# Optimization experiments

Hardware: AMD Instinct MI355X
Metric: run time of the kernel (lower is better)

The kernel has to match this reference:

```python
import jax, jax.numpy as jnp
import numpy as np

B, N, NC, D, H = 2, 8192, 512, 512, 16
HD = D // H            # 32
SCALE = HD ** -0.5
EPS = 1e-6


def setup_inputs() -> dict:
    key = jax.random.key(0)
    k0, k1, k2, k3, k4 = jax.random.split(key, 5)
    return {
        "x": jax.random.normal(k0, (B, N, D), dtype=jnp.float32),
        "clusters": jax.random.normal(k1, (B, NC, D), dtype=jnp.float32),
        "Wq": jax.random.normal(k2, (D, D), dtype=jnp.float32) * 0.02,
        "Wkv": jax.random.normal(k3, (D, 2 * D), dtype=jnp.float32) * 0.02,
        "Wout": jax.random.normal(k4, (D, D), dtype=jnp.float32) * 0.02,
    }


def reference(x, clusters, Wq, Wkv, Wout):
    # projections (torch Linear without bias == matmul with weight)
    q = clusters @ Wq                      # [b, nc, d]
    kv = x @ Wkv                           # [b, n, 2d]
    # split heads: 'b n (h d) -> b h n d' and 'b n (k h d) -> k b h n d'
    q = q.reshape(B, NC, H, HD).transpose(0, 2, 1, 3)        # [b, h, nc, hd]
    kv = kv.reshape(B, N, 2, H, HD)
    k = kv[:, :, 0].transpose(0, 2, 1, 3)                    # [b, h, n, hd]
    v = kv[:, :, 1].transpose(0, 2, 1, 3)                    # [b, h, n, hd]

    attn = jnp.einsum('bhqd,bhkd->bhqk', q, k) * SCALE       # [b, h, nc, n]
    # 'soft' assignment: softmax over the CLUSTER (query) axis, dim=-2
    attn = jax.nn.softmax(attn, axis=-2)
    token_sizes = attn.sum(-1)                               # [b, h, nc]
    attn = attn / (token_sizes[..., None] + EPS)
    token_sizes = token_sizes.mean(axis=1)                   # [b, nc]

    out = jnp.einsum('bhqk,bhkd->bhqd', attn, v)             # [b, h, nc, hd]
    out = out.transpose(0, 2, 1, 3).reshape(B, NC, D)        # [b, nc, d]
    out = out @ Wout
    return out, token_sizes
```

## Files before the change

kernel.cpp:

```cpp
#include <hip/hip_runtime.h>
#include <hip/hip_bf16.h>

#define B_ 2
#define N_ 8192
#define NC_ 512
#define D_ 512
#define H_ 16
#define HD_ 32
#define SCALE_ 0.17677669529663687f
#define LOG2E_ 1.4426950408889634f
#define EPS_ 1e-6f
#define NCHUNK 32
#define CHUNK (N_ / NCHUNK)

typedef __attribute__((ext_vector_type(8))) short bf16x8_t;
typedef __attribute__((ext_vector_type(4))) short bf16x4_t;
typedef __attribute__((ext_vector_type(4))) float f32x4_t;

static __device__ __forceinline__ short f2bf(float f) {
    unsigned u = __float_as_uint(f);
    unsigned r = (u + 0x7FFFu + ((u >> 16) & 1u)) >> 16;
    return (short)r;
}

static __device__ __forceinline__ float fast_exp2(float x) {
#if __has_builtin(__builtin_amdgcn_exp2f)
    return __builtin_amdgcn_exp2f(x);
#else
    float r; asm("v_exp_f32 %0, %1" : "=v"(r) : "v"(x)); return r;
#endif
}

static __device__ __forceinline__ void gload_lds16(const short* g, void* l) {
    __builtin_amdgcn_global_load_lds(
        (const __attribute__((address_space(1))) void*)g,
        (__attribute__((address_space(3))) void*)l, 16, 0, 0);
}

__global__ __launch_bounds__(256) void cvt_bf16_kernel(
    const float* __restrict__ a, short* __restrict__ ao, int na8,
    const float* __restrict__ b, short* __restrict__ bo)
{
    int i8 = blockIdx.x * 256 + threadIdx.x;
    const float* src; short* dst;
    if (i8 < na8) { src = a + (size_t)i8 * 8; dst = ao + (size_t)i8 * 8; }
    else { size_t o = (size_t)(i8 - na8) * 8; src = b + o; dst = bo + o; }
    float4 v0 = *(const float4*)src;
    float4 v1 = *(const float4*)(src + 4);
    bf16x8_t p = {f2bf(v0.x), f2bf(v0.y), f2bf(v0.z), f2bf(v0.w),
                  f2bf(v1.x), f2bf(v1.y), f2bf(v1.z), f2bf(v1.w)};
    *(bf16x8_t*)dst = p;
}

__global__ __launch_bounds__(256) void transpose_cvt_kernel(
    const float* __restrict__ Wq, const float* __restrict__ Wkv,
    const float* __restrict__ Wout,
    short* __restrict__ WqT, short* __restrict__ WkvT, short* __restrict__ WoutT)
{
    const float* src; short* dst; int ncols;
    if (blockIdx.z == 0)      { src = Wq;   dst = WqT;   ncols = 512; }
    else if (blockIdx.z == 1) { src = Wkv;  dst = WkvT;  ncols = 1024; }
    else                      { src = Wout; dst = WoutT; ncols = 512; }
    if ((int)blockIdx.x * 32 >= ncols) return;

    __shared__ short t[32][34];
    const int c0 = blockIdx.x * 32, r0 = blockIdx.y * 32;
    const int tc = threadIdx.x & 31, tr = threadIdx.x >> 5;
#pragma unroll
    for (int i = 0; i < 4; i++) {
        int r = tr + i * 8;
        t[tc][r] = f2bf(src[(size_t)(r0 + r) * ncols + c0 + tc]);
    }
    __syncthreads();
#pragma unroll
    for (int i = 0; i < 4; i++) {
        int outr = tr + i * 8;
        dst[(size_t)(c0 + outr) * 512 + r0 + tc] = t[outr][tc];
    }
}

template <bool OUT_BF16>
__global__ __launch_bounds__(256) void gemm_bt_kernel(
    const short* __restrict__ A, const short* __restrict__ BT,
    void* __restrict__ C, int M, int N, int K, float oscale)
{
    __shared__ short As[128 * 32];
    __shared__ short Bs[128 * 32];

    const int tid = threadIdx.x;
    const int wid = tid >> 6, lane = tid & 63;
    const int l16 = lane & 15, lg = lane >> 4;
    const int wr = (wid >> 1) * 64, wc = (wid & 1) * 64;

    const int nwg = gridDim.x * gridDim.y;
    const int flat = blockIdx.y * gridDim.x + blockIdx.x;
    const int swz = (flat & 7) * (nwg >> 3) + (flat >> 3);
    const int bx = swz % gridDim.x, by = swz / gridDim.x;

    const f32x4_t zero4 = {0.f, 0.f, 0.f, 0.f};
    f32x4_t acc[4][4];
#pragma unroll
    for (int i = 0; i < 4; i++)
#pragma unroll
        for (int j = 0; j < 4; j++) acc[i][j] = zero4;

    const short* aptr = A + (size_t)(by * 128 + wid * 16 + (lane >> 2)) * K + (lane & 3) * 8;
    const short* bptr = BT + (size_t)(bx * 128 + wid * 16 + (lane >> 2)) * K + (lane & 3) * 8;
    char* al = (char*)As + wid * 1024;
    char* bl = (char*)Bs + wid * 1024;
    const size_t rstep = (size_t)64 * K;

    for (int kt = 0; kt < K; kt += 32) {
        gload_lds16(aptr + kt, al);
        gload_lds16(aptr + rstep + kt, al + 4096);
        gload_lds16(bptr + kt, bl);
        gload_lds16(bptr + rstep + kt, bl + 4096);
        __syncthreads();

        bf16x8_t bfr[4];
#pragma unroll
        for (int nf = 0; nf < 4; nf++)
            bfr[nf] = *(const bf16x8_t*)&Bs[(wc + nf * 16 + l16) * 32 + lg * 8];
#pragma unroll
        for (int mf = 0; mf < 4; mf++) {
            bf16x8_t afr = *(const bf16x8_t*)&As[(wr + mf * 16 + l16) * 32 + lg * 8];
#pragma unroll
            for (int nf = 0; nf < 4; nf++)
                acc[mf][nf] = __builtin_amdgcn_mfma_f32_16x16x32_bf16(
                    afr, bfr[nf], acc[mf][nf], 0, 0, 0);
        }
        __syncthreads();
    }

#pragma unroll
    for (int mf = 0; mf < 4; mf++) {
#pragma unroll
        for (int nf = 0; nf < 4; nf++) {
            int row0 = by * 128 + wr + mf * 16 + lg * 4;
            int col  = bx * 128 + wc + nf * 16 + l16;
#pragma unroll
            for (int r = 0; r < 4; r++) {
                float v = acc[mf][nf][r] * oscale;
                if (OUT_BF16)
                    ((short*)C)[(size_t)(row0 + r) * N + col] = f2bf(v);
                else
                    ((float*)C)[(size_t)(row0 + r) * N + col] = v;
            }
        }
    }
}

__global__ __launch_bounds__(256) void attn_kernel(
    const short* __restrict__ qb,
    const short* __restrict__ kvb,
    short* __restrict__ out_part,
    float* __restrict__ ts_part)
{
    const int chunk = blockIdx.x, h = blockIdx.y, b = blockIdx.z;
    const int tid = threadIdx.x, wid = tid >> 6, lane = tid & 63;
    const int l16 = lane & 15, lg = lane >> 4;

    __shared__ short P_lds[512 * 32];
    __shared__ short v_t[2][32][40];
    __shared__ float reds[2][2][4][16];

    bf16x8_t qf[8];
#pragma unroll
    for (int mf = 0; mf < 8; mf++) {
        int row = wid * 128 + mf * 16 + l16;
        qf[mf] = *(const bf16x8_t*)&qb[(size_t)(b * NC_ + row) * D_ + h * HD_ + lg * 8];
    }

    const f32x4_t zero4 = {0.f, 0.f, 0.f, 0.f};
    f32x4_t oacc[8][2], tsacc[8];
#pragma unroll
    for (int mf = 0; mf < 8; mf++) {
        oacc[mf][0] = zero4; oacc[mf][1] = zero4; tsacc[mf] = zero4;
    }
    bf16x8_t onesf;
#pragma unroll
    for (int j = 0; j < 8; j++) onesf[j] = (short)0x3F80;

    const short* kptr = kvb + (size_t)(b * N_ + chunk * CHUNK + l16) * (2 * D_) + h * HD_ + lg * 8;
    const int skey = tid >> 3, sd0 = (tid & 7) * 4;
    const short* vptr = kvb + (size_t)(b * N_ + chunk * CHUNK + skey) * (2 * D_) + D_ + h * HD_ + sd0;
    char* Pb = (char*)P_lds;

    for (int kt = 0; kt < CHUNK / 32; kt++) {
        const int cur = kt & 1;
        const size_t koff = (size_t)kt * 32 * (2 * D_);

        bf16x8_t kf0 = *(const bf16x8_t*)(kptr + koff);
        bf16x8_t kf1 = *(const bf16x8_t*)(kptr + koff + 16 * (2 * D_));
        bf16x4_t vv  = *(const bf16x4_t*)(vptr + koff);
        v_t[cur][sd0 + 0][skey] = vv[0];
        v_t[cur][sd0 + 1][skey] = vv[1];
        v_t[cur][sd0 + 2][skey] = vv[2];
        v_t[cur][sd0 + 3][skey] = vv[3];

#pragma unroll
        for (int half = 0; half < 2; half++) {
            f32x4_t s[8];
            bf16x8_t kf = half ? kf1 : kf0;
#pragma unroll
            for (int mf = 0; mf < 8; mf++)
                s[mf] = __builtin_amdgcn_mfma_f32_16x16x32_bf16(qf[mf], kf, zero4, 0, 0, 0);

            float sl = 0.f;
#pragma unroll
            for (int mf = 0; mf < 8; mf++)
#pragma unroll
                for (int r = 0; r < 4; r++) {
                    float e = fast_exp2(s[mf][r]);
                    s[mf][r] = e; sl += e;
                }
            sl += __shfl_xor(sl, 16, 64);
            sl += __shfl_xor(sl, 32, 64);
            if (lane < 16) reds[cur][half][wid][lane] = sl;
            __syncthreads();
            float inv = __fdividef(1.f, reds[cur][half][0][l16] + reds[cur][half][1][l16] +
                                        reds[cur][half][2][l16] + reds[cur][half][3][l16]);

            const int kbyte = (l16 & 7) * 2;
            const int ku = (l16 >> 3) + half * 2;
#pragma unroll
            for (int mf = 0; mf < 8; mf++) {
#pragma unroll
                for (int r = 0; r < 4; r++) {
                    int row = wid * 128 + mf * 16 + lg * 4 + r;
                    int x = (row >> 1) & 3;
                    int by0 = row * 64 + kbyte + (((ku ^ x) & 3) << 4);
                    *(short*)(Pb + by0) = (short)(__float_as_uint(s[mf][r] * inv) >> 16);
                }
            }
        }

        bf16x8_t v0 = *(const bf16x8_t*)&v_t[cur][l16][lg * 8];
        bf16x8_t v1 = *(const bf16x8_t*)&v_t[cur][16 + l16][lg * 8];
#pragma unroll
        for (int mf = 0; mf < 8; mf++) {
            int row = wid * 128 + mf * 16 + l16;
            bf16x8_t pa = *(const bf16x8_t*)(Pb + row * 64 +
                              (((lg ^ ((row >> 1) & 3)) & 3) << 4));
            oacc[mf][0] = __builtin_amdgcn_mfma_f32_16x16x32_bf16(pa, v0, oacc[mf][0], 0, 0, 0);
            oacc[mf][1] = __builtin_amdgcn_mfma_f32_16x16x32_bf16(pa, v1, oacc[mf][1], 0, 0, 0);
            tsacc[mf]   = __builtin_amdgcn_mfma_f32_16x16x32_bf16(pa, onesf, tsacc[mf], 0, 0, 0);
        }
    }

    const size_t base = ((size_t)(chunk * B_ + b) * H_ + h);
#pragma unroll
    for (int mf = 0; mf < 8; mf++) {
        int row0 = wid * 128 + mf * 16 + lg * 4;
#pragma unroll
        for (int nf = 0; nf < 2; nf++) {
            int col = nf * 16 + l16;
#pragma unroll
            for (int r = 0; r < 4; r++)
                out_part[(base * NC_ + row0 + r) * HD_ + col] = f2bf(oacc[mf][nf][r]);
        }
        if (l16 == 0) {
#pragma unroll
            for (int r = 0; r < 4; r++)
                ts_part[base * NC_ + row0 + r] = tsacc[mf][r];
        }
    }
}

__global__ __launch_bounds__(256) void reduce_kernel(
    const short* __restrict__ out_part, const float* __restrict__ ts_part,
    short* __restrict__ out_mid, float* __restrict__ tok_out)
{
    const int bnc = blockIdx.x;
    const int b = bnc >> 9, nc = bnc & 511;
    const int t = threadIdx.x;
    __shared__ float tsh[16];
    if (t < 16) {
        float s = 0.f;
#pragma unroll
        for (int ch = 0; ch < NCHUNK; ch++)
            s += ts_part[((size_t)(ch * B_ + b) * H_ + t) * NC_ + nc];
        tsh[t] = s;
    }
    __syncthreads();
    if (t == 0) {
        float s = 0.f;
#pragma unroll
        for (int i = 0; i < 16; i++) s += tsh[i];
        tok_out[b * NC_ + nc] = s * (1.f / 16.f);
    }
    for (int c = t; c < D_; c += 256) {
        int hh = c >> 5, d = c & 31;
        float s = 0.f;
#pragma unroll
        for (int ch = 0; ch < NCHUNK; ch++) {
            unsigned short u = (unsigned short)
                out_part[(((size_t)(ch * B_ + b) * H_ + hh) * NC_ + nc) * HD_ + d];
            s += __uint_as_float((unsigned)u << 16);
        }
        out_mid[(size_t)(b * NC_ + nc) * D_ + c] = f2bf(s / (tsh[hh] + EPS_));
    }
}

extern "C" void kernel_launch(void* const* d_in, const int* in_sizes, int n_in,
                              void* d_out, int out_size, void* d_ws, size_t ws_size,
                              hipStream_t stream)
{
    (void)in_sizes; (void)n_in; (void)out_size; (void)ws_size;
    const float* x        = (const float*)d_in[0];
    const float* clusters = (const float*)d_in[1];
    const float* Wq       = (const float*)d_in[2];
    const float* Wkv      = (const float*)d_in[3];
    const float* Wout     = (const float*)d_in[4];

    char* ws = (char*)d_ws;
    short* x_bf     = (short*)(ws);
    short* WkvT     = (short*)(ws + 16777216);
    short* cl_bf    = (short*)(ws + 17825792);
    short* WqT      = (short*)(ws + 18874368);
    short* out_part = (short*)(ws);
    float* ts_part  = (float*)(ws + 33554432);
    short* kvb      = (short*)(ws + 35651584);
    short* out_mid  = (short*)(ws + 35651584);
    short* qb       = (short*)(ws + 69206016);
    short* WoutT    = (short*)(ws + 70254592);

    float* out = (float*)d_out;
    float* tok = out + (size_t)B_ * NC_ * D_;

    cvt_bf16_kernel<<<dim3(4352), dim3(256), 0, stream>>>(
        x, x_bf, (B_ * N_ * D_) / 8, clusters, cl_bf);
    transpose_cvt_kernel<<<dim3(32, 16, 3), dim3(256), 0, stream>>>(
        Wq, Wkv, Wout, WqT, WkvT, WoutT);
    gemm_bt_kernel<true><<<dim3((2 * D_) / 128, (B_ * N_) / 128), dim3(256), 0, stream>>>(
        x_bf, WkvT, kvb, B_ * N_, 2 * D_, D_, 1.0f);
    gemm_bt_kernel<true><<<dim3(D_ / 128, (B_ * NC_) / 128), dim3(256), 0, stream>>>(
        cl_bf, WqT, qb, B_ * NC_, D_, D_, SCALE_ * LOG2E_);
    attn_kernel<<<dim3(NCHUNK, H_, B_), dim3(256), 0, stream>>>(
        qb, kvb, out_part, ts_part);
    reduce_kernel<<<dim3(B_ * NC_), dim3(256), 0, stream>>>(
        out_part, ts_part, out_mid, tok);
    gemm_bt_kernel<false><<<dim3(D_ / 128, (B_ * NC_) / 128), dim3(256), 0, stream>>>(
        out_mid, WoutT, d_out, B_ * NC_, D_, D_, 1.0f);
}
```

Baseline: 137.2 us.

## Keep softmax probabilities in registers and feed PV MFMA directly via transposed S

Computes S transposed (K as A operand) so each lane holds four consecutive keys for one query. The normalized probabilities are packed straight into bf16x4 operands for 16x16x16 MFMAs against V, which removes the P round-trip through LDS. Token sizes are now accumulated with scalar adds instead of an MFMA with a ones vector, and outputs are stored as packed truncated bf16. In exchange the column sums need more shuffles, the kernel uses smaller MFMAs, and it rounds by truncation instead of round-to-nearest.

```diff
diff --git a/kernel.cpp b/kernel.cpp
--- a/kernel.cpp
+++ b/kernel.cpp
@@ -16,6 +16,7 @@
 typedef __attribute__((ext_vector_type(8))) short bf16x8_t;
 typedef __attribute__((ext_vector_type(4))) short bf16x4_t;
 typedef __attribute__((ext_vector_type(4))) float f32x4_t;
+typedef __attribute__((ext_vector_type(2))) unsigned int u32x2_t;
 
 static __device__ __forceinline__ short f2bf(float f) {
     unsigned u = __float_as_uint(f);
@@ -28,6 +29,27 @@
     return __builtin_amdgcn_exp2f(x);
 #else
     float r; asm("v_exp_f32 %0, %1" : "=v"(r) : "v"(x)); return r;
+#endif
+}
+
+static __device__ __forceinline__ unsigned pack_trunc(float lo, float hi) {
+    return __builtin_amdgcn_perm(__float_as_uint(hi), __float_as_uint(lo), 0x07060302u);
+}
+
+static __device__ __forceinline__ bf16x4_t as_bf16x4(unsigned u0, unsigned u1) {
+    union { u32x2_t u; bf16x4_t v; } x;
+    x.u[0] = u0; x.u[1] = u1;
+    return x.v;
+}
+
+static __device__ __forceinline__ f32x4_t mfma16(bf16x4_t a, bf16x4_t b, f32x4_t c) {
+#if __has_builtin(__builtin_amdgcn_mfma_f32_16x16x16bf16_1k)
+    return __builtin_amdgcn_mfma_f32_16x16x16bf16_1k(a, b, c, 0, 0, 0);
+#else
+    f32x4_t d;
+    asm volatile("v_mfma_f32_16x16x16_bf16 %0, %1, %2, %3"
+                 : "=&v"(d) : "v"(a), "v"(b), "v"(c));
+    return d;
 #endif
 }
 
@@ -160,7 +182,6 @@
     const int tid = threadIdx.x, wid = tid >> 6, lane = tid & 63;
     const int l16 = lane & 15, lg = lane >> 4;
 
-    __shared__ short P_lds[512 * 32];
     __shared__ short v_t[2][32][40];
     __shared__ float reds[2][2][4][16];
 
@@ -172,98 +193,94 @@
     }
 
     const f32x4_t zero4 = {0.f, 0.f, 0.f, 0.f};
-    f32x4_t oacc[8][2], tsacc[8];
+    f32x4_t oacc[8][2];
+    float tsp[8];
 #pragma unroll
     for (int mf = 0; mf < 8; mf++) {
-        oacc[mf][0] = zero4; oacc[mf][1] = zero4; tsacc[mf] = zero4;
-    }
-    bf16x8_t onesf;
-#pragma unroll
-    for (int j = 0; j < 8; j++) onesf[j] = (short)0x3F80;
+        oacc[mf][0] = zero4; oacc[mf][1] = zero4; tsp[mf] = 0.f;
+    }
 
     const short* kptr = kvb + (size_t)(b * N_ + chunk * CHUNK + l16) * (2 * D_) + h * HD_ + lg * 8;
     const int skey = tid >> 3, sd0 = (tid & 7) * 4;
     const short* vptr = kvb + (size_t)(b * N_ + chunk * CHUNK + skey) * (2 * D_) + D_ + h * HD_ + sd0;
-    char* Pb = (char*)P_lds;
 
     for (int kt = 0; kt < CHUNK / 32; kt++) {
         const int cur = kt & 1;
         const size_t koff = (size_t)kt * 32 * (2 * D_);
 
-        bf16x8_t kf0 = *(const bf16x8_t*)(kptr + koff);
-        bf16x8_t kf1 = *(const bf16x8_t*)(kptr + koff + 16 * (2 * D_));
-        bf16x4_t vv  = *(const bf16x4_t*)(vptr + koff);
+        bf16x4_t vv = *(const bf16x4_t*)(vptr + koff);
         v_t[cur][sd0 + 0][skey] = vv[0];
         v_t[cur][sd0 + 1][skey] = vv[1];
         v_t[cur][sd0 + 2][skey] = vv[2];
         v_t[cur][sd0 + 3][skey] = vv[3];
-
-#pragma unroll
-        for (int half = 0; half < 2; half++) {
+        bf16x8_t kf0 = *(const bf16x8_t*)(kptr + koff);
+        bf16x8_t kf1 = *(const bf16x8_t*)(kptr + koff + 16 * (2 * D_));
+
+#pragma unroll
+        for (int hf = 0; hf < 2; hf++) {
+            bf16x8_t kf = hf ? kf1 : kf0;
             f32x4_t s[8];
-            bf16x8_t kf = half ? kf1 : kf0;
 #pragma unroll
             for (int mf = 0; mf < 8; mf++)
-                s[mf] = __builtin_amdgcn_mfma_f32_16x16x32_bf16(qf[mf], kf, zero4, 0, 0, 0);
-
-            float sl = 0.f;
-#pragma unroll
-            for (int mf = 0; mf < 8; mf++)
-#pragma unroll
-                for (int r = 0; r < 4; r++) {
-                    float e = fast_exp2(s[mf][r]);
-                    s[mf][r] = e; sl += e;
-                }
-            sl += __shfl_xor(sl, 16, 64);
-            sl += __shfl_xor(sl, 32, 64);
-            if (lane < 16) reds[cur][half][wid][lane] = sl;
+                s[mf] = __builtin_amdgcn_mfma_f32_16x16x32_bf16(kf, qf[mf], zero4, 0, 0, 0);
+
+            f32x4_t csum = zero4;
+#pragma unroll
+            for (int mf = 0; mf < 8; mf++) {
+#pragma unroll
+                for (int r = 0; r < 4; r++) s[mf][r] = fast_exp2(s[mf][r]);
+                csum += s[mf];
+            }
+#pragma unroll
+            for (int m = 1; m <= 8; m <<= 1) {
+#pragma unroll
+                for (int r = 0; r < 4; r++) csum[r] += __shfl_xor(csum[r], m, 64);
+            }
+            if (l16 == 0) {
+                reds[cur][hf][wid][lg * 4 + 0] = csum[0];
+                reds[cur][hf][wid][lg * 4 + 1] = csum[1];
+                reds[cur][hf][wid][lg * 4 + 2] = csum[2];
+                reds[cur][hf][wid][lg * 4 + 3] = csum[3];
+            }
             __syncthreads();
-            float inv = __fdividef(1.f, reds[cur][half][0][l16] + reds[cur][half][1][l16] +
-                                        reds[cur][half][2][l16] + reds[cur][half][3][l16]);
-
-            const int kbyte = (l16 & 7) * 2;
-            const int ku = (l16 >> 3) + half * 2;
+            f32x4_t tot = *(const f32x4_t*)&reds[cur][hf][0][lg * 4];
+            tot += *(const f32x4_t*)&reds[cur][hf][1][lg * 4];
+            tot += *(const f32x4_t*)&reds[cur][hf][2][lg * 4];
+            tot += *(const f32x4_t*)&reds[cur][hf][3][lg * 4];
+            f32x4_t inv;
+#pragma unroll
+            for (int r = 0; r < 4; r++) inv[r] = __fdividef(1.f, tot[r]);
+
+            bf16x4_t va0 = *(const bf16x4_t*)&v_t[cur][l16][hf * 16 + lg * 4];
+            bf16x4_t va1 = *(const bf16x4_t*)&v_t[cur][16 + l16][hf * 16 + lg * 4];
+
 #pragma unroll
             for (int mf = 0; mf < 8; mf++) {
-#pragma unroll
-                for (int r = 0; r < 4; r++) {
-                    int row = wid * 128 + mf * 16 + lg * 4 + r;
-                    int x = (row >> 1) & 3;
-                    int by0 = row * 64 + kbyte + (((ku ^ x) & 3) << 4);
-                    *(short*)(Pb + by0) = (short)(__float_as_uint(s[mf][r] * inv) >> 16);
-                }
-            }
-        }
-
-        bf16x8_t v0 = *(const bf16x8_t*)&v_t[cur][l16][lg * 8];
-        bf16x8_t v1 = *(const bf16x8_t*)&v_t[cur][16 + l16][lg * 8];
-#pragma unroll
-        for (int mf = 0; mf < 8; mf++) {
-            int row = wid * 128 + mf * 16 + l16;
-            bf16x8_t pa = *(const bf16x8_t*)(Pb + row * 64 +
-                              (((lg ^ ((row >> 1) & 3)) & 3) << 4));
-            oacc[mf][0] = __builtin_amdgcn_mfma_f32_16x16x32_bf16(pa, v0, oacc[mf][0], 0, 0, 0);
-            oacc[mf][1] = __builtin_amdgcn_mfma_f32_16x16x32_bf16(pa, v1, oacc[mf][1], 0, 0, 0);
-            tsacc[mf]   = __builtin_amdgcn_mfma_f32_16x16x32_bf16(pa, onesf, tsacc[mf], 0, 0, 0);
+                float t0 = s[mf][0] * inv[0], t1 = s[mf][1] * inv[1];
+                float t2 = s[mf][2] * inv[2], t3 = s[mf][3] * inv[3];
+                tsp[mf] += (t0 + t1) + (t2 + t3);
+                bf16x4_t pa = as_bf16x4(pack_trunc(t0, t1), pack_trunc(t2, t3));
+                oacc[mf][0] = mfma16(va0, pa, oacc[mf][0]);
+                oacc[mf][1] = mfma16(va1, pa, oacc[mf][1]);
+            }
         }
     }
 
     const size_t base = ((size_t)(chunk * B_ + b) * H_ + h);
 #pragma unroll
     for (int mf = 0; mf < 8; mf++) {
-        int row0 = wid * 128 + mf * 16 + lg * 4;
-#pragma unroll
-        for (int nf = 0; nf < 2; nf++) {
-            int col = nf * 16 + l16;
-#pragma unroll
-            for (int r = 0; r < 4; r++)
-                out_part[(base * NC_ + row0 + r) * HD_ + col] = f2bf(oacc[mf][nf][r]);
-        }
-        if (l16 == 0) {
-#pragma unroll
-            for (int r = 0; r < 4; r++)
-                ts_part[base * NC_ + row0 + r] = tsacc[mf][r];
-        }
+        int q = wid * 128 + mf * 16 + l16;
+#pragma unroll
+        for (int dh = 0; dh < 2; dh++) {
+            u32x2_t po;
+            po[0] = pack_trunc(oacc[mf][dh][0], oacc[mf][dh][1]);
+            po[1] = pack_trunc(oacc[mf][dh][2], oacc[mf][dh][3]);
+            *(u32x2_t*)&out_part[(base * NC_ + q) * HD_ + dh * 16 + lg * 4] = po;
+        }
+        float t = tsp[mf];
+        t += __shfl_xor(t, 16, 64);
+        t += __shfl_xor(t, 32, 64);
+        if (lg == 0) ts_part[base * NC_ + q] = t;
     }
 }
 
```

After: 141.7 us. 3.2% more time.

## Fold softmax column normalization into V operand and merge barriers per tile

Applied to the files above, without the earlier changes.

Unnormalized exponentials go straight to LDS in bf16. The per-key 1/colsum is applied to the V fragment and to a reciprocal vector that replaces the ones vector in the token-size MFMA. This removes one of the two block barriers per 32-key tile and the separate normalize-and-store pass. Next-tile K/V global loads are issued before the barrier to overlap latency. The cost is different bf16 rounding (truncation of V*inv and of the reciprocals), which may shift accuracy.

```diff
diff --git a/kernel.cpp b/kernel.cpp
--- a/kernel.cpp
+++ b/kernel.cpp
@@ -31,6 +31,14 @@
 #endif
 }
 
+static __device__ __forceinline__ unsigned pack_trunc(float lo, float hi) {
+    return __builtin_amdgcn_perm(__float_as_uint(hi), __float_as_uint(lo), 0x07060302u);
+}
+
+static __device__ __forceinline__ float bf2f(short s) {
+    return __uint_as_float((unsigned)(unsigned short)s << 16);
+}
+
 static __device__ __forceinline__ void gload_lds16(const short* g, void* l) {
     __builtin_amdgcn_global_load_lds(
         (const __attribute__((address_space(1))) void*)g,
@@ -162,7 +170,7 @@
 
     __shared__ short P_lds[512 * 32];
     __shared__ short v_t[2][32][40];
-    __shared__ float reds[2][2][4][16];
+    __shared__ float reds[2][4][32];
 
     bf16x8_t qf[8];
 #pragma unroll
@@ -177,22 +185,19 @@
     for (int mf = 0; mf < 8; mf++) {
         oacc[mf][0] = zero4; oacc[mf][1] = zero4; tsacc[mf] = zero4;
     }
-    bf16x8_t onesf;
-#pragma unroll
-    for (int j = 0; j < 8; j++) onesf[j] = (short)0x3F80;
 
     const short* kptr = kvb + (size_t)(b * N_ + chunk * CHUNK + l16) * (2 * D_) + h * HD_ + lg * 8;
     const int skey = tid >> 3, sd0 = (tid & 7) * 4;
     const short* vptr = kvb + (size_t)(b * N_ + chunk * CHUNK + skey) * (2 * D_) + D_ + h * HD_ + sd0;
     char* Pb = (char*)P_lds;
 
+    bf16x8_t kf0 = *(const bf16x8_t*)(kptr);
+    bf16x8_t kf1 = *(const bf16x8_t*)(kptr + 16 * (2 * D_));
+    bf16x4_t vv  = *(const bf16x4_t*)(vptr);
+
     for (int kt = 0; kt < CHUNK / 32; kt++) {
         const int cur = kt & 1;
-        const size_t koff = (size_t)kt * 32 * (2 * D_);
-
-        bf16x8_t kf0 = *(const bf16x8_t*)(kptr + koff);
-        bf16x8_t kf1 = *(const bf16x8_t*)(kptr + koff + 16 * (2 * D_));
-        bf16x4_t vv  = *(const bf16x4_t*)(vptr + koff);
+
         v_t[cur][sd0 + 0][skey] = vv[0];
         v_t[cur][sd0 + 1][skey] = vv[1];
         v_t[cur][sd0 + 2][skey] = vv[2];
@@ -206,37 +211,68 @@
             for (int mf = 0; mf < 8; mf++)
                 s[mf] = __builtin_amdgcn_mfma_f32_16x16x32_bf16(qf[mf], kf, zero4, 0, 0, 0);
 
+            const int kbyte = (l16 & 7) * 2;
+            const int ku = (l16 >> 3) + half * 2;
             float sl = 0.f;
 #pragma unroll
-            for (int mf = 0; mf < 8; mf++)
+            for (int mf = 0; mf < 8; mf++) {
 #pragma unroll
                 for (int r = 0; r < 4; r++) {
                     float e = fast_exp2(s[mf][r]);
-                    s[mf][r] = e; sl += e;
+                    sl += e;
+                    int row = wid * 128 + mf * 16 + lg * 4 + r;
+                    int x = (row >> 1) & 3;
+                    *(short*)(Pb + row * 64 + kbyte + (((ku ^ x) & 3) << 4)) =
+                        (short)(__float_as_uint(e) >> 16);
                 }
+            }
             sl += __shfl_xor(sl, 16, 64);
             sl += __shfl_xor(sl, 32, 64);
-            if (lane < 16) reds[cur][half][wid][lane] = sl;
-            __syncthreads();
-            float inv = __fdividef(1.f, reds[cur][half][0][l16] + reds[cur][half][1][l16] +
-                                        reds[cur][half][2][l16] + reds[cur][half][3][l16]);
-
-            const int kbyte = (l16 & 7) * 2;
-            const int ku = (l16 >> 3) + half * 2;
-#pragma unroll
-            for (int mf = 0; mf < 8; mf++) {
-#pragma unroll
-                for (int r = 0; r < 4; r++) {
-                    int row = wid * 128 + mf * 16 + lg * 4 + r;
-                    int x = (row >> 1) & 3;
-                    int by0 = row * 64 + kbyte + (((ku ^ x) & 3) << 4);
-                    *(short*)(Pb + by0) = (short)(__float_as_uint(s[mf][r] * inv) >> 16);
-                }
+            if (lane < 16) reds[cur][wid][half * 16 + lane] = sl;
+        }
+
+        {
+            const size_t koffn = (size_t)((kt + 1) & (CHUNK / 32 - 1)) * 32 * (2 * D_);
+            kf0 = *(const bf16x8_t*)(kptr + koffn);
+            kf1 = *(const bf16x8_t*)(kptr + koffn + 16 * (2 * D_));
+            vv  = *(const bf16x4_t*)(vptr + koffn);
+        }
+
+        __syncthreads();
+
+        f32x4_t ta = *(const f32x4_t*)&reds[cur][0][lg * 8];
+        f32x4_t tb = *(const f32x4_t*)&reds[cur][0][lg * 8 + 4];
+#pragma unroll
+        for (int w = 1; w < 4; w++) {
+            ta += *(const f32x4_t*)&reds[cur][w][lg * 8];
+            tb += *(const f32x4_t*)&reds[cur][w][lg * 8 + 4];
+        }
+        float iv[8];
+#pragma unroll
+        for (int r = 0; r < 4; r++) {
+            iv[r]     = __fdividef(1.f, ta[r]);
+            iv[4 + r] = __fdividef(1.f, tb[r]);
+        }
+
+        bf16x8_t v0r = *(const bf16x8_t*)&v_t[cur][l16][lg * 8];
+        bf16x8_t v1r = *(const bf16x8_t*)&v_t[cur][16 + l16][lg * 8];
+        bf16x8_t v0, v1, invf;
+        {
+            unsigned* p0 = (unsigned*)&v0;
+            unsigned* p1 = (unsigned*)&v1;
+            unsigned* pi = (unsigned*)&invf;
+#pragma unroll
+            for (int j = 0; j < 4; j++) {
+                float a0 = bf2f(v0r[2 * j])     * iv[2 * j];
+                float a1 = bf2f(v0r[2 * j + 1]) * iv[2 * j + 1];
+                float b0 = bf2f(v1r[2 * j])     * iv[2 * j];
+                float b1 = bf2f(v1r[2 * j + 1]) * iv[2 * j + 1];
+                p0[j] = pack_trunc(a0, a1);
+                p1[j] = pack_trunc(b0, b1);
+                pi[j] = pack_trunc(iv[2 * j], iv[2 * j + 1]);
             }
         }
 
-        bf16x8_t v0 = *(const bf16x8_t*)&v_t[cur][l16][lg * 8];
-        bf16x8_t v1 = *(const bf16x8_t*)&v_t[cur][16 + l16][lg * 8];
 #pragma unroll
         for (int mf = 0; mf < 8; mf++) {
             int row = wid * 128 + mf * 16 + l16;
@@ -244,7 +280,7 @@
                               (((lg ^ ((row >> 1) & 3)) & 3) << 4));
             oacc[mf][0] = __builtin_amdgcn_mfma_f32_16x16x32_bf16(pa, v0, oacc[mf][0], 0, 0, 0);
             oacc[mf][1] = __builtin_amdgcn_mfma_f32_16x16x32_bf16(pa, v1, oacc[mf][1], 0, 0, 0);
-            tsacc[mf]   = __builtin_amdgcn_mfma_f32_16x16x32_bf16(pa, onesf, tsacc[mf], 0, 0, 0);
+            tsacc[mf]   = __builtin_amdgcn_mfma_f32_16x16x32_bf16(pa, invf, tsacc[mf], 0, 0, 0);
         }
     }
 
```

Measured after the change: 133.6 us. -2.6%, faster.
